# Kernel tuning notes

Hardware: AMD Instinct MI355X
Metric: run time of the kernel (lower is better)

Reference implementation:

```python
import jax, jax.numpy as jnp
import numpy as np

B, C, H, W = 8, 192, 128, 128
FILTERS = (1, 3, 3, 3, 3, 1)
BOUND = 1e-9


def setup_inputs() -> dict:
    key = jax.random.key(0)
    ks = jax.random.split(key, 16)
    d = {"x": jax.random.normal(ks[0], (B, C, H, W), jnp.float32)}
    for i in range(5):
        d[f"m{i}"] = jax.random.normal(ks[1 + i], (C, FILTERS[i + 1], FILTERS[i]), jnp.float32) * 0.5
        d[f"b{i}"] = jax.random.uniform(ks[6 + i], (C, FILTERS[i + 1], 1), jnp.float32, -0.5, 0.5)
    for i in range(4):
        d[f"f{i}"] = jax.random.normal(ks[11 + i], (C, FILTERS[i + 1], 1), jnp.float32) * 0.1
    return d


def _logits_cumulative(x, ms, bs, fs):
    # x: (C, 1, N); per-channel tiny MLP: matmul(softplus(M), x) + b, tanh gate
    logits = x
    for i in range(5):
        logits = jnp.matmul(jax.nn.softplus(ms[i]), logits) + bs[i]
        if i < 4:
            logits = logits + jnp.tanh(fs[i]) * jnp.tanh(logits)
    return logits


def reference(x, m0, m1, m2, m3, m4, b0, b1, b2, b3, b4, f0, f1, f2, f3):
    ms = (m0, m1, m2, m3, m4)
    bs = (b0, b1, b2, b3, b4)
    fs = (f0, f1, f2, f3)
    # quantize: per-sample min/max over (C,H,W), round to 16-bit grid
    x_min = jnp.min(x, axis=(1, 2, 3), keepdims=True)
    x_max = jnp.max(x, axis=(1, 2, 3), keepdims=True)
    xq = jnp.round((x - x_min) * 65535.0 / (x_max - x_min + 1e-12))
    xd = xq / 65535.0  # dequantize
    # permute (B,C,H,W)->(C,B,H,W), reshape to (C,1,N)
    xp = jnp.transpose(xd, (1, 0, 2, 3)).reshape(C, 1, -1)
    lower = _logits_cumulative(xp - 0.5, ms, bs, fs)
    upper = _logits_cumulative(xp + 0.5, ms, bs, fs)
    likelihood = jax.nn.sigmoid(upper) - jax.nn.sigmoid(lower)
    likelihood = jnp.maximum(likelihood, BOUND)  # LowerBound forward
    x_out = jnp.transpose(xp.reshape(C, B, H, W), (1, 0, 2, 3))
    likelihood = jnp.transpose(likelihood.reshape(C, B, H, W), (1, 0, 2, 3))
    return (x_out, likelihood)
```

## Files before the change

### kernel.cpp

```cpp
#include <hip/hip_runtime.h>
#include <math.h>

#define CCH 192
#define BATCH 8
#define HWSZ 16384
#define NPER (CCH * HWSZ)
#define NTOT ((size_t)BATCH * NPER)
#define INV65535 (1.0f / 65535.0f)

#define TABN    8193
#define TABSTR  8196
#define TSCALE  (8192.0f / 65535.0f)

#define WS_PMN_OFF_FLOATS  64
#define WS_PMX_OFF_FLOATS  2048
#define WS_WTAB_OFF_FLOATS 4096
#define WS_TAB_OFF_BYTES   65536
#define WS_NEEDED (WS_TAB_OFF_BYTES + (size_t)CCH * TABSTR * 4)

#define RED_BLOCKS_PER_SAMPLE 192
#define MINMAX_BLOCKS (BATCH * RED_BLOCKS_PER_SAMPLE)
#define TAB_BLOCKS (CCH * 33)

typedef float f4 __attribute__((ext_vector_type(4)));

__device__ __forceinline__ float fexp2(float x) { return __builtin_amdgcn_exp2f(x); }
__device__ __forceinline__ float frcp(float x)  { return __builtin_amdgcn_rcpf(x); }
__device__ __forceinline__ float ftanh(float x) {
    return 1.0f - 2.0f * frcp(fexp2(2.8853900817779268f * x) + 1.0f);
}
__device__ __forceinline__ float fsig(float x) {
    return frcp(1.0f + fexp2(-1.4426950408889634f * x));
}

__device__ __forceinline__ float eval_mlp(float x, const float* W)
{
    float a0 = fmaf(W[0], x, W[33]);
    float a1 = fmaf(W[1], x, W[34]);
    float a2 = fmaf(W[2], x, W[35]);
    a0 = fmaf(W[46], ftanh(a0), a0);
    a1 = fmaf(W[47], ftanh(a1), a1);
    a2 = fmaf(W[48], ftanh(a2), a2);

    float c0 = fmaf(W[3], a0, fmaf(W[4],  a1, fmaf(W[5],  a2, W[36])));
    float c1 = fmaf(W[6], a0, fmaf(W[7],  a1, fmaf(W[8],  a2, W[37])));
    float c2 = fmaf(W[9], a0, fmaf(W[10], a1, fmaf(W[11], a2, W[38])));
    c0 = fmaf(W[49], ftanh(c0), c0);
    c1 = fmaf(W[50], ftanh(c1), c1);
    c2 = fmaf(W[51], ftanh(c2), c2);

    float d0 = fmaf(W[12], c0, fmaf(W[13], c1, fmaf(W[14], c2, W[39])));
    float d1 = fmaf(W[15], c0, fmaf(W[16], c1, fmaf(W[17], c2, W[40])));
    float d2 = fmaf(W[18], c0, fmaf(W[19], c1, fmaf(W[20], c2, W[41])));
    d0 = fmaf(W[52], ftanh(d0), d0);
    d1 = fmaf(W[53], ftanh(d1), d1);
    d2 = fmaf(W[54], ftanh(d2), d2);

    float e0 = fmaf(W[21], d0, fmaf(W[22], d1, fmaf(W[23], d2, W[42])));
    float e1 = fmaf(W[24], d0, fmaf(W[25], d1, fmaf(W[26], d2, W[43])));
    float e2 = fmaf(W[27], d0, fmaf(W[28], d1, fmaf(W[29], d2, W[44])));
    e0 = fmaf(W[55], ftanh(e0), e0);
    e1 = fmaf(W[56], ftanh(e1), e1);
    e2 = fmaf(W[57], ftanh(e2), e2);

    return fmaf(W[30], e0, fmaf(W[31], e1, fmaf(W[32], e2, W[45])));
}

__device__ __forceinline__ float eval_lik(float d, const float* W)
{
    float lo = eval_mlp(d - 0.5f, W);
    float up = eval_mlp(d + 0.5f, W);
    return fmaxf(fsig(up) - fsig(lo), 1e-9f);
}

__device__ __forceinline__ void minmax_block(const float* __restrict__ x,
                                             float* __restrict__ pmn,
                                             float* __restrict__ pmx,
                                             int bid)
{
    int b   = bid / RED_BLOCKS_PER_SAMPLE;
    int blk = bid % RED_BLOCKS_PER_SAMPLE;
    const f4* xs = (const f4*)(x + (size_t)b * NPER);
    int base = blk * 4096;
    float mn = INFINITY, mx = -INFINITY;
    #pragma unroll
    for (int i = 0; i < 16; ++i) {
        f4 v = xs[base + i * 256 + threadIdx.x];
        mn = fminf(mn, fminf(fminf(v.x, v.y), fminf(v.z, v.w)));
        mx = fmaxf(mx, fmaxf(fmaxf(v.x, v.y), fmaxf(v.z, v.w)));
    }
    #pragma unroll
    for (int off = 32; off > 0; off >>= 1) {
        mn = fminf(mn, __shfl_down(mn, off, 64));
        mx = fmaxf(mx, __shfl_down(mx, off, 64));
    }
    __shared__ float smn[4], smx[4];
    int wave = threadIdx.x >> 6;
    if ((threadIdx.x & 63) == 0) { smn[wave] = mn; smx[wave] = mx; }
    __syncthreads();
    if (threadIdx.x == 0) {
        #pragma unroll
        for (int i = 1; i < 4; ++i) { mn = fminf(mn, smn[i]); mx = fmaxf(mx, smx[i]); }
        pmn[bid] = mn;
        pmx[bid] = mx;
    }
}

__global__ __launch_bounds__(256) void prep_kernel(
    const float* __restrict__ x,
    float* __restrict__ pmn, float* __restrict__ pmx,
    const float* __restrict__ m0, const float* __restrict__ b0,
    const float* __restrict__ m1, const float* __restrict__ b1,
    const float* __restrict__ m2, const float* __restrict__ b2,
    const float* __restrict__ m3, const float* __restrict__ b3,
    const float* __restrict__ m4, const float* __restrict__ b4,
    const float* __restrict__ f0, const float* __restrict__ f1,
    const float* __restrict__ f2, const float* __restrict__ f3,
    float* __restrict__ tab)
{
    if (blockIdx.x < MINMAX_BLOCKS) {
        minmax_block(x, pmn, pmx, blockIdx.x);
        return;
    }
    int tb = blockIdx.x - MINMAX_BLOCKS;
    int c  = tb / 33;
    int jc = tb % 33;
    int t  = threadIdx.x;

    __shared__ float sW[58];
    if (t < 58) {
        float v;
        if (t < 33) {
            if      (t < 3)  v = m0[c * 3 + t];
            else if (t < 12) v = m1[c * 9 + t - 3];
            else if (t < 21) v = m2[c * 9 + t - 12];
            else if (t < 30) v = m3[c * 9 + t - 21];
            else             v = m4[c * 3 + t - 30];
            v = fmaxf(v, 0.f) + log1pf(expf(-fabsf(v)));
        } else if (t < 46) {
            int i = t - 33;
            if      (i < 3)  v = b0[c * 3 + i];
            else if (i < 6)  v = b1[c * 3 + i - 3];
            else if (i < 9)  v = b2[c * 3 + i - 6];
            else if (i < 12) v = b3[c * 3 + i - 9];
            else             v = b4[c];
        } else {
            int i = t - 46;
            if      (i < 3)  v = f0[c * 3 + i];
            else if (i < 6)  v = f1[c * 3 + i - 3];
            else if (i < 9)  v = f2[c * 3 + i - 6];
            else             v = f3[c * 3 + i - 9];
            v = tanhf(v);
        }
        sW[t] = v;
    }
    __syncthreads();

    float W[58];
    #pragma unroll
    for (int i = 0; i < 58; ++i) W[i] = sW[i];

    int j = jc * 256 + t;
    if (j < TABN) {
        float d = (float)j * (1.0f / 8192.0f);
        tab[(size_t)c * TABSTR + j] = eval_lik(d, W);
    }
}

__global__ __launch_bounds__(256) void gather_kernel(const float* __restrict__ x,
                                                     const float* __restrict__ pmn,
                                                     const float* __restrict__ pmx,
                                                     const float* __restrict__ tab,
                                                     float* __restrict__ out)
{
    __shared__ __align__(16) float ltab[TABN + 3];
    __shared__ float red[4][4];

    int c  = blockIdx.x >> 2;
    int p  = blockIdx.x & 3;
    int b0 = p;
    int b1 = p + 4;
    int t  = threadIdx.x;

    size_t base0 = ((size_t)b0 * CCH + c) * HWSZ;
    size_t base1 = ((size_t)b1 * CCH + c) * HWSZ;
    const f4* xin0 = (const f4*)(x + base0);
    const f4* xin1 = (const f4*)(x + base1);

    f4 pf0 = __builtin_nontemporal_load(&xin0[t]);
    f4 pf1 = __builtin_nontemporal_load(&xin1[t]);

    const f4* tsrc = (const f4*)(tab + (size_t)c * TABSTR);
    f4* tdst = (f4*)ltab;
    #pragma unroll
    for (int i = 0; i < 8; ++i) tdst[i * 256 + t] = tsrc[i * 256 + t];
    if (t == 0) ltab[8192] = tab[(size_t)c * TABSTR + 8192];

    float mn0 = t < 192 ? pmn[b0 * RED_BLOCKS_PER_SAMPLE + t] :  INFINITY;
    float mx0 = t < 192 ? pmx[b0 * RED_BLOCKS_PER_SAMPLE + t] : -INFINITY;
    float mn1 = t < 192 ? pmn[b1 * RED_BLOCKS_PER_SAMPLE + t] :  INFINITY;
    float mx1 = t < 192 ? pmx[b1 * RED_BLOCKS_PER_SAMPLE + t] : -INFINITY;
    #pragma unroll
    for (int off = 32; off > 0; off >>= 1) {
        mn0 = fminf(mn0, __shfl_down(mn0, off, 64));
        mx0 = fmaxf(mx0, __shfl_down(mx0, off, 64));
        mn1 = fminf(mn1, __shfl_down(mn1, off, 64));
        mx1 = fmaxf(mx1, __shfl_down(mx1, off, 64));
    }
    int wave = t >> 6;
    if ((t & 63) == 0) {
        red[wave][0] = mn0; red[wave][1] = mx0;
        red[wave][2] = mn1; red[wave][3] = mx1;
    }
    __syncthreads();

    mn0 = fminf(fminf(red[0][0], red[1][0]), fminf(red[2][0], red[3][0]));
    mx0 = fmaxf(fmaxf(red[0][1], red[1][1]), fmaxf(red[2][1], red[3][1]));
    mn1 = fminf(fminf(red[0][2], red[1][2]), fminf(red[2][2], red[3][2]));
    mx1 = fmaxf(fmaxf(red[0][3], red[1][3]), fmaxf(red[2][3], red[3][3]));
    float scale0 = 65535.0f / (mx0 - mn0 + 1e-12f);
    float scale1 = 65535.0f / (mx1 - mn1 + 1e-12f);

    auto proc = [&](float xi, float mn, float scale, float& od, float& ol) {
        float kf   = rintf((xi - mn) * scale);
        od         = kf * INV65535;
        float tpos = kf * TSCALE;
        int   j    = (int)tpos;
        j = j > 8191 ? 8191 : j;
        float frac = tpos - (float)j;
        float t0 = ltab[j];
        float t1 = ltab[j + 1];
        ol = fmaxf(fmaf(frac, t1 - t0, t0), 1e-9f);
    };

    auto plane = [&](const f4* xin, f4* o0, f4* o1, float mn, float scale, f4 pf) {
        #pragma unroll
        for (int i = 0; i < 16; ++i) {
            f4 v = (i == 0) ? pf : __builtin_nontemporal_load(&xin[i * 256 + t]);
            float in[4] = {v.x, v.y, v.z, v.w};
            float xd[4], lk[4];
            #pragma unroll
            for (int k = 0; k < 4; ++k) proc(in[k], mn, scale, xd[k], lk[k]);
            f4 vxd = {xd[0], xd[1], xd[2], xd[3]};
            f4 vlk = {lk[0], lk[1], lk[2], lk[3]};
            __builtin_nontemporal_store(vxd, &o0[i * 256 + t]);
            __builtin_nontemporal_store(vlk, &o1[i * 256 + t]);
        }
    };

    plane(xin0, (f4*)(out + base0), (f4*)(out + NTOT + base0), mn0, scale0, pf0);
    plane(xin1, (f4*)(out + base1), (f4*)(out + NTOT + base1), mn1, scale1, pf1);
}

__global__ void setup_kernel(const float* __restrict__ m0, const float* __restrict__ b0,
                             const float* __restrict__ m1, const float* __restrict__ b1,
                             const float* __restrict__ m2, const float* __restrict__ b2,
                             const float* __restrict__ m3, const float* __restrict__ b3,
                             const float* __restrict__ m4, const float* __restrict__ b4,
                             const float* __restrict__ f0, const float* __restrict__ f1,
                             const float* __restrict__ f2, const float* __restrict__ f3,
                             float* __restrict__ wtab)
{
    int t = threadIdx.x;
    if (t < CCH) {
        float* w = wtab + t * 64;
        #pragma unroll
        for (int i = 0; i < 3; ++i) { float v = m0[t*3+i]; w[i]    = fmaxf(v,0.f)+log1pf(expf(-fabsf(v))); }
        #pragma unroll
        for (int i = 0; i < 9; ++i) { float v = m1[t*9+i]; w[3+i]  = fmaxf(v,0.f)+log1pf(expf(-fabsf(v))); }
        #pragma unroll
        for (int i = 0; i < 9; ++i) { float v = m2[t*9+i]; w[12+i] = fmaxf(v,0.f)+log1pf(expf(-fabsf(v))); }
        #pragma unroll
        for (int i = 0; i < 9; ++i) { float v = m3[t*9+i]; w[21+i] = fmaxf(v,0.f)+log1pf(expf(-fabsf(v))); }
        #pragma unroll
        for (int i = 0; i < 3; ++i) { float v = m4[t*3+i]; w[30+i] = fmaxf(v,0.f)+log1pf(expf(-fabsf(v))); }
        #pragma unroll
        for (int i = 0; i < 3; ++i) w[33+i] = b0[t*3+i];
        #pragma unroll
        for (int i = 0; i < 3; ++i) w[36+i] = b1[t*3+i];
        #pragma unroll
        for (int i = 0; i < 3; ++i) w[39+i] = b2[t*3+i];
        #pragma unroll
        for (int i = 0; i < 3; ++i) w[42+i] = b3[t*3+i];
        w[45] = b4[t];
        #pragma unroll
        for (int i = 0; i < 3; ++i) w[46+i] = tanhf(f0[t*3+i]);
        #pragma unroll
        for (int i = 0; i < 3; ++i) w[49+i] = tanhf(f1[t*3+i]);
        #pragma unroll
        for (int i = 0; i < 3; ++i) w[52+i] = tanhf(f2[t*3+i]);
        #pragma unroll
        for (int i = 0; i < 3; ++i) w[55+i] = tanhf(f3[t*3+i]);
    }
}

__global__ __launch_bounds__(256) void ebott_main(const float* __restrict__ x,
                                                  const float* __restrict__ pmn,
                                                  const float* __restrict__ pmx,
                                                  const float* __restrict__ wtab,
                                                  float* __restrict__ out)
{
    int blk = blockIdx.x;
    int q   = blk & 3;
    int c   = (blk >> 2) % CCH;
    int b   = blk / (4 * CCH);

    float W[58];
    const float* w = wtab + c * 64;
    #pragma unroll
    for (int i = 0; i < 58; ++i) W[i] = w[i];

    float mn = INFINITY, mx = -INFINITY;
    for (int i = 0; i < RED_BLOCKS_PER_SAMPLE; ++i) {
        mn = fminf(mn, pmn[b * RED_BLOCKS_PER_SAMPLE + i]);
        mx = fmaxf(mx, pmx[b * RED_BLOCKS_PER_SAMPLE + i]);
    }
    float scale = 65535.0f / (mx - mn + 1e-12f);

    size_t base = (size_t)(b * CCH + c) * HWSZ + q * 4096;
    const f4* xin = (const f4*)(x + base);
    f4* o0 = (f4*)(out + base);
    f4* o1 = (f4*)(out + NTOT + base);
    int t = threadIdx.x;

    #pragma unroll
    for (int i = 0; i < 4; ++i) {
        f4 v = xin[i * 256 + t];
        float in[4] = {v.x, v.y, v.z, v.w};
        float xd[4], lk[4];
        #pragma unroll
        for (int k = 0; k < 4; ++k) {
            float d = rintf((in[k] - mn) * scale) * INV65535;
            xd[k] = d;
            lk[k] = eval_lik(d, W);
        }
        f4 vxd = {xd[0], xd[1], xd[2], xd[3]};
        f4 vlk = {lk[0], lk[1], lk[2], lk[3]};
        o0[i * 256 + t] = vxd;
        o1[i * 256 + t] = vlk;
    }
}

extern "C" void kernel_launch(void* const* d_in, const int* in_sizes, int n_in,
                              void* d_out, int out_size, void* d_ws, size_t ws_size,
                              hipStream_t stream)
{
    const float* x  = (const float*)d_in[0];
    const float* m0 = (const float*)d_in[1];
    const float* b0 = (const float*)d_in[2];
    const float* m1 = (const float*)d_in[3];
    const float* b1 = (const float*)d_in[4];
    const float* m2 = (const float*)d_in[5];
    const float* b2 = (const float*)d_in[6];
    const float* m3 = (const float*)d_in[7];
    const float* b3 = (const float*)d_in[8];
    const float* m4 = (const float*)d_in[9];
    const float* b4 = (const float*)d_in[10];
    const float* f0 = (const float*)d_in[11];
    const float* f1 = (const float*)d_in[12];
    const float* f2 = (const float*)d_in[13];
    const float* f3 = (const float*)d_in[14];

    float* pmn  = (float*)d_ws + WS_PMN_OFF_FLOATS;
    float* pmx  = (float*)d_ws + WS_PMX_OFF_FLOATS;
    float* wtab = (float*)d_ws + WS_WTAB_OFF_FLOATS;
    float* tab  = (float*)((char*)d_ws + WS_TAB_OFF_BYTES);
    float* out  = (float*)d_out;

    if (ws_size >= WS_NEEDED) {
        prep_kernel<<<MINMAX_BLOCKS + TAB_BLOCKS, 256, 0, stream>>>(
            x, pmn, pmx, m0, b0, m1, b1, m2, b2, m3, b3, m4, b4, f0, f1, f2, f3, tab);
        gather_kernel<<<CCH * 4, 256, 0, stream>>>(x, pmn, pmx, tab, out);
    } else {
        setup_kernel<<<1, 256, 0, stream>>>(m0, b0, m1, b1, m2, b2, m3, b3, m4, b4,
                                            f0, f1, f2, f3, wtab);
        prep_kernel<<<MINMAX_BLOCKS, 256, 0, stream>>>(
            x, pmn, pmx, m0, b0, m1, b1, m2, b2, m3, b3, m4, b4, f0, f1, f2, f3, tab);
        ebott_main<<<BATCH * CCH * 4, 256, 0, stream>>>(x, pmn, pmx, wtab, out);
    }
}
```

Before: 324.3 us.

## Fuse minmax, table build and gather into one cooperative kernel with grid sync

Replaces the two-kernel scheme (prep with minmax plus global table, then gather) with a single cooperative kernel. Each block builds its channel's likelihood table directly in LDS while reducing min/max over its own planes, then a grid-wide sync makes the per-sample extrema visible before the gather. This removes the global table round-trip and one launch, and overlaps table evaluation with the minmax read pass. The cost is a grid barrier and reduced occupancy limits; a two-kernel fallback is kept for devices without cooperative launch.

```diff
diff --git a/kernel.cpp b/kernel.cpp
--- a/kernel.cpp
+++ b/kernel.cpp
@@ -1,5 +1,8 @@
 #include <hip/hip_runtime.h>
+#include <hip/hip_cooperative_groups.h>
 #include <math.h>
+
+namespace cg = cooperative_groups;
 
 #define CCH 192
 #define BATCH 8
@@ -9,18 +12,13 @@
 #define INV65535 (1.0f / 65535.0f)
 
 #define TABN    8193
-#define TABSTR  8196
 #define TSCALE  (8192.0f / 65535.0f)
 
-#define WS_PMN_OFF_FLOATS  64
-#define WS_PMX_OFF_FLOATS  2048
-#define WS_WTAB_OFF_FLOATS 4096
-#define WS_TAB_OFF_BYTES   65536
-#define WS_NEEDED (WS_TAB_OFF_BYTES + (size_t)CCH * TABSTR * 4)
-
-#define RED_BLOCKS_PER_SAMPLE 192
-#define MINMAX_BLOCKS (BATCH * RED_BLOCKS_PER_SAMPLE)
-#define TAB_BLOCKS (CCH * 33)
+#define WS_PMN_OFF 64
+#define WS_PMX_OFF 2112
+#define WS_NEEDED  ((size_t)(WS_PMX_OFF + BATCH * CCH) * 4)
+
+#define NBLK (CCH * 4)
 
 typedef float f4 __attribute__((ext_vector_type(4)));
 
@@ -73,61 +71,15 @@
     return fmaxf(fsig(up) - fsig(lo), 1e-9f);
 }
 
-__device__ __forceinline__ void minmax_block(const float* __restrict__ x,
-                                             float* __restrict__ pmn,
-                                             float* __restrict__ pmx,
-                                             int bid)
-{
-    int b   = bid / RED_BLOCKS_PER_SAMPLE;
-    int blk = bid % RED_BLOCKS_PER_SAMPLE;
-    const f4* xs = (const f4*)(x + (size_t)b * NPER);
-    int base = blk * 4096;
-    float mn = INFINITY, mx = -INFINITY;
-    #pragma unroll
-    for (int i = 0; i < 16; ++i) {
-        f4 v = xs[base + i * 256 + threadIdx.x];
-        mn = fminf(mn, fminf(fminf(v.x, v.y), fminf(v.z, v.w)));
-        mx = fmaxf(mx, fmaxf(fmaxf(v.x, v.y), fmaxf(v.z, v.w)));
-    }
-    #pragma unroll
-    for (int off = 32; off > 0; off >>= 1) {
-        mn = fminf(mn, __shfl_down(mn, off, 64));
-        mx = fmaxf(mx, __shfl_down(mx, off, 64));
-    }
-    __shared__ float smn[4], smx[4];
-    int wave = threadIdx.x >> 6;
-    if ((threadIdx.x & 63) == 0) { smn[wave] = mn; smx[wave] = mx; }
-    __syncthreads();
-    if (threadIdx.x == 0) {
-        #pragma unroll
-        for (int i = 1; i < 4; ++i) { mn = fminf(mn, smn[i]); mx = fmaxf(mx, smx[i]); }
-        pmn[bid] = mn;
-        pmx[bid] = mx;
-    }
-}
-
-__global__ __launch_bounds__(256) void prep_kernel(
-    const float* __restrict__ x,
-    float* __restrict__ pmn, float* __restrict__ pmx,
+__device__ __forceinline__ void stage_weights(int c, int t, float* sW,
     const float* __restrict__ m0, const float* __restrict__ b0,
     const float* __restrict__ m1, const float* __restrict__ b1,
     const float* __restrict__ m2, const float* __restrict__ b2,
     const float* __restrict__ m3, const float* __restrict__ b3,
     const float* __restrict__ m4, const float* __restrict__ b4,
     const float* __restrict__ f0, const float* __restrict__ f1,
-    const float* __restrict__ f2, const float* __restrict__ f3,
-    float* __restrict__ tab)
-{
-    if (blockIdx.x < MINMAX_BLOCKS) {
-        minmax_block(x, pmn, pmx, blockIdx.x);
-        return;
-    }
-    int tb = blockIdx.x - MINMAX_BLOCKS;
-    int c  = tb / 33;
-    int jc = tb % 33;
-    int t  = threadIdx.x;
-
-    __shared__ float sW[58];
+    const float* __restrict__ f2, const float* __restrict__ f3)
+{
     if (t < 58) {
         float v;
         if (t < 33) {
@@ -154,52 +106,128 @@
         }
         sW[t] = v;
     }
-    __syncthreads();
-
-    float W[58];
-    #pragma unroll
-    for (int i = 0; i < 58; ++i) W[i] = sW[i];
-
-    int j = jc * 256 + t;
-    if (j < TABN) {
-        float d = (float)j * (1.0f / 8192.0f);
-        tab[(size_t)c * TABSTR + j] = eval_lik(d, W);
-    }
-}
-
-__global__ __launch_bounds__(256) void gather_kernel(const float* __restrict__ x,
-                                                     const float* __restrict__ pmn,
-                                                     const float* __restrict__ pmx,
-                                                     const float* __restrict__ tab,
-                                                     float* __restrict__ out)
-{
-    __shared__ __align__(16) float ltab[TABN + 3];
-    __shared__ float red[4][4];
-
-    int c  = blockIdx.x >> 2;
-    int p  = blockIdx.x & 3;
-    int b0 = p;
-    int b1 = p + 4;
-    int t  = threadIdx.x;
-
-    size_t base0 = ((size_t)b0 * CCH + c) * HWSZ;
-    size_t base1 = ((size_t)b1 * CCH + c) * HWSZ;
+}
+
+__device__ __forceinline__ void gather_plane(const f4* __restrict__ xin,
+                                             f4* __restrict__ o0, f4* __restrict__ o1,
+                                             float mn, float scale,
+                                             const float* ltab, int t, f4 pf)
+{
+    #pragma unroll
+    for (int i = 0; i < 16; ++i) {
+        f4 v = (i == 0) ? pf : xin[i * 256 + t];
+        float in[4] = {v.x, v.y, v.z, v.w};
+        float xd[4], lk[4];
+        #pragma unroll
+        for (int k = 0; k < 4; ++k) {
+            float kf   = rintf((in[k] - mn) * scale);
+            xd[k]      = kf * INV65535;
+            float tpos = kf * TSCALE;
+            int   j    = (int)tpos;
+            j = j > 8191 ? 8191 : j;
+            float frac = tpos - (float)j;
+            float t0 = ltab[j];
+            float t1 = ltab[j + 1];
+            lk[k] = fmaxf(fmaf(frac, t1 - t0, t0), 1e-9f);
+        }
+        f4 vxd = {xd[0], xd[1], xd[2], xd[3]};
+        f4 vlk = {lk[0], lk[1], lk[2], lk[3]};
+        __builtin_nontemporal_store(vxd, &o0[i * 256 + t]);
+        __builtin_nontemporal_store(vlk, &o1[i * 256 + t]);
+    }
+}
+
+__device__ __forceinline__ void phase2_gather(
+    const float* __restrict__ x, const float* __restrict__ pmn,
+    const float* __restrict__ pmx, float* __restrict__ out,
+    const float* ltab, float (*red)[4], int c, int p, int t)
+{
+    int s0 = p, s1 = p + 4;
+    size_t base0 = ((size_t)s0 * CCH + c) * HWSZ;
+    size_t base1 = ((size_t)s1 * CCH + c) * HWSZ;
     const f4* xin0 = (const f4*)(x + base0);
     const f4* xin1 = (const f4*)(x + base1);
 
-    f4 pf0 = __builtin_nontemporal_load(&xin0[t]);
-    f4 pf1 = __builtin_nontemporal_load(&xin1[t]);
-
-    const f4* tsrc = (const f4*)(tab + (size_t)c * TABSTR);
-    f4* tdst = (f4*)ltab;
-    #pragma unroll
-    for (int i = 0; i < 8; ++i) tdst[i * 256 + t] = tsrc[i * 256 + t];
-    if (t == 0) ltab[8192] = tab[(size_t)c * TABSTR + 8192];
-
-    float mn0 = t < 192 ? pmn[b0 * RED_BLOCKS_PER_SAMPLE + t] :  INFINITY;
-    float mx0 = t < 192 ? pmx[b0 * RED_BLOCKS_PER_SAMPLE + t] : -INFINITY;
-    float mn1 = t < 192 ? pmn[b1 * RED_BLOCKS_PER_SAMPLE + t] :  INFINITY;
-    float mx1 = t < 192 ? pmx[b1 * RED_BLOCKS_PER_SAMPLE + t] : -INFINITY;
+    f4 pf0 = xin0[t];
+    f4 pf1 = xin1[t];
+
+    float amn0 = t < CCH ? pmn[s0 * CCH + t] :  INFINITY;
+    float amx0 = t < CCH ? pmx[s0 * CCH + t] : -INFINITY;
+    float amn1 = t < CCH ? pmn[s1 * CCH + t] :  INFINITY;
+    float amx1 = t < CCH ? pmx[s1 * CCH + t] : -INFINITY;
+    #pragma unroll
+    for (int off = 32; off > 0; off >>= 1) {
+        amn0 = fminf(amn0, __shfl_down(amn0, off, 64));
+        amx0 = fmaxf(amx0, __shfl_down(amx0, off, 64));
+        amn1 = fminf(amn1, __shfl_down(amn1, off, 64));
+        amx1 = fmaxf(amx1, __shfl_down(amx1, off, 64));
+    }
+    int wave = t >> 6;
+    if ((t & 63) == 0) {
+        red[wave][0] = amn0; red[wave][1] = amx0;
+        red[wave][2] = amn1; red[wave][3] = amx1;
+    }
+    __syncthreads();
+    float mn0 = fminf(fminf(red[0][0], red[1][0]), fminf(red[2][0], red[3][0]));
+    float mx0 = fmaxf(fmaxf(red[0][1], red[1][1]), fmaxf(red[2][1], red[3][1]));
+    float mn1 = fminf(fminf(red[0][2], red[1][2]), fminf(red[2][2], red[3][2]));
+    float mx1 = fmaxf(fmaxf(red[0][3], red[1][3]), fmaxf(red[2][3], red[3][3]));
+    float sc0 = 65535.0f / (mx0 - mn0 + 1e-12f);
+    float sc1 = 65535.0f / (mx1 - mn1 + 1e-12f);
+
+    gather_plane(xin0, (f4*)(out + base0), (f4*)(out + NTOT + base0), mn0, sc0, ltab, t, pf0);
+    gather_plane(xin1, (f4*)(out + base1), (f4*)(out + NTOT + base1), mn1, sc1, ltab, t, pf1);
+}
+
+__global__ __launch_bounds__(256, 3) void fused_kernel(
+    const float* __restrict__ x,
+    float* __restrict__ pmn, float* __restrict__ pmx,
+    float* __restrict__ out,
+    const float* __restrict__ m0, const float* __restrict__ b0,
+    const float* __restrict__ m1, const float* __restrict__ b1,
+    const float* __restrict__ m2, const float* __restrict__ b2,
+    const float* __restrict__ m3, const float* __restrict__ b3,
+    const float* __restrict__ m4, const float* __restrict__ b4,
+    const float* __restrict__ f0, const float* __restrict__ f1,
+    const float* __restrict__ f2, const float* __restrict__ f3)
+{
+    __shared__ __align__(16) float ltab[TABN + 3];
+    __shared__ float sW[58];
+    __shared__ float red[4][4];
+
+    int c = blockIdx.x >> 2;
+    int p = blockIdx.x & 3;
+    int s0 = p, s1 = p + 4;
+    int t = threadIdx.x;
+
+    stage_weights(c, t, sW, m0, b0, m1, b1, m2, b2, m3, b3, m4, b4, f0, f1, f2, f3);
+    __syncthreads();
+
+    float W[58];
+    #pragma unroll
+    for (int i = 0; i < 58; ++i) W[i] = sW[i];
+
+    size_t base0 = ((size_t)s0 * CCH + c) * HWSZ;
+    size_t base1 = ((size_t)s1 * CCH + c) * HWSZ;
+    const f4* xin0 = (const f4*)(x + base0);
+    const f4* xin1 = (const f4*)(x + base1);
+
+    float mn0 = INFINITY, mx0 = -INFINITY, mn1 = INFINITY, mx1 = -INFINITY;
+
+    #pragma unroll 2
+    for (int it = 0; it < 16; ++it) {
+        f4 v0 = xin0[it * 256 + t];
+        f4 v1 = xin1[it * 256 + t];
+        int j = it * 512 + t;
+        ltab[j]       = eval_lik((float)j * (1.0f / 8192.0f), W);
+        ltab[j + 256] = eval_lik((float)(j + 256) * (1.0f / 8192.0f), W);
+        mn0 = fminf(mn0, fminf(fminf(v0.x, v0.y), fminf(v0.z, v0.w)));
+        mx0 = fmaxf(mx0, fmaxf(fmaxf(v0.x, v0.y), fmaxf(v0.z, v0.w)));
+        mn1 = fminf(mn1, fminf(fminf(v1.x, v1.y), fminf(v1.z, v1.w)));
+        mx1 = fmaxf(mx1, fmaxf(fmaxf(v1.x, v1.y), fmaxf(v1.z, v1.w)));
+    }
+    if (t == 0) ltab[8192] = eval_lik(1.0f, W);
+
     #pragma unroll
     for (int off = 32; off > 0; off >>= 1) {
         mn0 = fminf(mn0, __shfl_down(mn0, off, 64));
@@ -213,132 +241,86 @@
         red[wave][2] = mn1; red[wave][3] = mx1;
     }
     __syncthreads();
-
-    mn0 = fminf(fminf(red[0][0], red[1][0]), fminf(red[2][0], red[3][0]));
-    mx0 = fmaxf(fmaxf(red[0][1], red[1][1]), fmaxf(red[2][1], red[3][1]));
-    mn1 = fminf(fminf(red[0][2], red[1][2]), fminf(red[2][2], red[3][2]));
-    mx1 = fmaxf(fmaxf(red[0][3], red[1][3]), fmaxf(red[2][3], red[3][3]));
-    float scale0 = 65535.0f / (mx0 - mn0 + 1e-12f);
-    float scale1 = 65535.0f / (mx1 - mn1 + 1e-12f);
-
-    auto proc = [&](float xi, float mn, float scale, float& od, float& ol) {
-        float kf   = rintf((xi - mn) * scale);
-        od         = kf * INV65535;
-        float tpos = kf * TSCALE;
-        int   j    = (int)tpos;
-        j = j > 8191 ? 8191 : j;
-        float frac = tpos - (float)j;
-        float t0 = ltab[j];
-        float t1 = ltab[j + 1];
-        ol = fmaxf(fmaf(frac, t1 - t0, t0), 1e-9f);
-    };
-
-    auto plane = [&](const f4* xin, f4* o0, f4* o1, float mn, float scale, f4 pf) {
+    if (t == 0) {
         #pragma unroll
-        for (int i = 0; i < 16; ++i) {
-            f4 v = (i == 0) ? pf : __builtin_nontemporal_load(&xin[i * 256 + t]);
-            float in[4] = {v.x, v.y, v.z, v.w};
-            float xd[4], lk[4];
-            #pragma unroll
-            for (int k = 0; k < 4; ++k) proc(in[k], mn, scale, xd[k], lk[k]);
-            f4 vxd = {xd[0], xd[1], xd[2], xd[3]};
-            f4 vlk = {lk[0], lk[1], lk[2], lk[3]};
-            __builtin_nontemporal_store(vxd, &o0[i * 256 + t]);
-            __builtin_nontemporal_store(vlk, &o1[i * 256 + t]);
+        for (int i = 1; i < 4; ++i) {
+            mn0 = fminf(mn0, red[i][0]); mx0 = fmaxf(mx0, red[i][1]);
+            mn1 = fminf(mn1, red[i][2]); mx1 = fmaxf(mx1, red[i][3]);
         }
-    };
-
-    plane(xin0, (f4*)(out + base0), (f4*)(out + NTOT + base0), mn0, scale0, pf0);
-    plane(xin1, (f4*)(out + base1), (f4*)(out + NTOT + base1), mn1, scale1, pf1);
-}
-
-__global__ void setup_kernel(const float* __restrict__ m0, const float* __restrict__ b0,
-                             const float* __restrict__ m1, const float* __restrict__ b1,
-                             const float* __restrict__ m2, const float* __restrict__ b2,
-                             const float* __restrict__ m3, const float* __restrict__ b3,
-                             const float* __restrict__ m4, const float* __restrict__ b4,
-                             const float* __restrict__ f0, const float* __restrict__ f1,
-                             const float* __restrict__ f2, const float* __restrict__ f3,
-                             float* __restrict__ wtab)
-{
+        pmn[s0 * CCH + c] = mn0; pmx[s0 * CCH + c] = mx0;
+        pmn[s1 * CCH + c] = mn1; pmx[s1 * CCH + c] = mx1;
+    }
+    __threadfence();
+    cg::this_grid().sync();
+
+    phase2_gather(x, pmn, pmx, out, ltab, red, c, p, t);
+}
+
+__global__ __launch_bounds__(256) void minmax_kernel(const float* __restrict__ x,
+                                                     float* __restrict__ pmn,
+                                                     float* __restrict__ pmx)
+{
+    const f4* xs = (const f4*)(x + (size_t)blockIdx.x * HWSZ);
     int t = threadIdx.x;
-    if (t < CCH) {
-        float* w = wtab + t * 64;
+    float mn = INFINITY, mx = -INFINITY;
+    #pragma unroll
+    for (int i = 0; i < 16; ++i) {
+        f4 v = xs[i * 256 + t];
+        mn = fminf(mn, fminf(fminf(v.x, v.y), fminf(v.z, v.w)));
+        mx = fmaxf(mx, fmaxf(fmaxf(v.x, v.y), fmaxf(v.z, v.w)));
+    }
+    #pragma unroll
+    for (int off = 32; off > 0; off >>= 1) {
+        mn = fminf(mn, __shfl_down(mn, off, 64));
+        mx = fmaxf(mx, __shfl_down(mx, off, 64));
+    }
+    __shared__ float smn[4], smx[4];
+    int wave = t >> 6;
+    if ((t & 63) == 0) { smn[wave] = mn; smx[wave] = mx; }
+    __syncthreads();
+    if (t == 0) {
         #pragma unroll
-        for (int i = 0; i < 3; ++i) { float v = m0[t*3+i]; w[i]    = fmaxf(v,0.f)+log1pf(expf(-fabsf(v))); }
-        #pragma unroll
-        for (int i = 0; i < 9; ++i) { float v = m1[t*9+i]; w[3+i]  = fmaxf(v,0.f)+log1pf(expf(-fabsf(v))); }
-        #pragma unroll
-        for (int i = 0; i < 9; ++i) { float v = m2[t*9+i]; w[12+i] = fmaxf(v,0.f)+log1pf(expf(-fabsf(v))); }
-        #pragma unroll
-        for (int i = 0; i < 9; ++i) { float v = m3[t*9+i]; w[21+i] = fmaxf(v,0.f)+log1pf(expf(-fabsf(v))); }
-        #pragma unroll
-        for (int i = 0; i < 3; ++i) { float v = m4[t*3+i]; w[30+i] = fmaxf(v,0.f)+log1pf(expf(-fabsf(v))); }
-        #pragma unroll
-        for (int i = 0; i < 3; ++i) w[33+i] = b0[t*3+i];
-        #pragma unroll
-        for (int i = 0; i < 3; ++i) w[36+i] = b1[t*3+i];
-        #pragma unroll
-        for (int i = 0; i < 3; ++i) w[39+i] = b2[t*3+i];
-        #pragma unroll
-        for (int i = 0; i < 3; ++i) w[42+i] = b3[t*3+i];
-        w[45] = b4[t];
-        #pragma unroll
-        for (int i = 0; i < 3; ++i) w[46+i] = tanhf(f0[t*3+i]);
-        #pragma unroll
-        for (int i = 0; i < 3; ++i) w[49+i] = tanhf(f1[t*3+i]);
-        #pragma unroll
-        for (int i = 0; i < 3; ++i) w[52+i] = tanhf(f2[t*3+i]);
-        #pragma unroll
-        for (int i = 0; i < 3; ++i) w[55+i] = tanhf(f3[t*3+i]);
-    }
-}
-
-__global__ __launch_bounds__(256) void ebott_main(const float* __restrict__ x,
-                                                  const float* __restrict__ pmn,
-                                                  const float* __restrict__ pmx,
-                                                  const float* __restrict__ wtab,
-                                                  float* __restrict__ out)
-{
-    int blk = blockIdx.x;
-    int q   = blk & 3;
-    int c   = (blk >> 2) % CCH;
-    int b   = blk / (4 * CCH);
+        for (int i = 1; i < 4; ++i) { mn = fminf(mn, smn[i]); mx = fmaxf(mx, smx[i]); }
+        pmn[blockIdx.x] = mn;
+        pmx[blockIdx.x] = mx;
+    }
+}
+
+__global__ __launch_bounds__(256, 3) void gather_local_kernel(
+    const float* __restrict__ x,
+    const float* __restrict__ pmn, const float* __restrict__ pmx,
+    const float* __restrict__ m0, const float* __restrict__ b0,
+    const float* __restrict__ m1, const float* __restrict__ b1,
+    const float* __restrict__ m2, const float* __restrict__ b2,
+    const float* __restrict__ m3, const float* __restrict__ b3,
+    const float* __restrict__ m4, const float* __restrict__ b4,
+    const float* __restrict__ f0, const float* __restrict__ f1,
+    const float* __restrict__ f2, const float* __restrict__ f3,
+    float* __restrict__ out)
+{
+    __shared__ __align__(16) float ltab[TABN + 3];
+    __shared__ float sW[58];
+    __shared__ float red[4][4];
+
+    int c = blockIdx.x >> 2;
+    int p = blockIdx.x & 3;
+    int t = threadIdx.x;
+
+    stage_weights(c, t, sW, m0, b0, m1, b1, m2, b2, m3, b3, m4, b4, f0, f1, f2, f3);
+    __syncthreads();
 
     float W[58];
-    const float* w = wtab + c * 64;
-    #pragma unroll
-    for (int i = 0; i < 58; ++i) W[i] = w[i];
-
-    float mn = INFINITY, mx = -INFINITY;
-    for (int i = 0; i < RED_BLOCKS_PER_SAMPLE; ++i) {
-        mn = fminf(mn, pmn[b * RED_BLOCKS_PER_SAMPLE + i]);
-        mx = fmaxf(mx, pmx[b * RED_BLOCKS_PER_SAMPLE + i]);
-    }
-    float scale = 65535.0f / (mx - mn + 1e-12f);
-
-    size_t base = (size_t)(b * CCH + c) * HWSZ + q * 4096;
-    const f4* xin = (const f4*)(x + base);
-    f4* o0 = (f4*)(out + base);
-    f4* o1 = (f4*)(out + NTOT + base);
-    int t = threadIdx.x;
-
-    #pragma unroll
-    for (int i = 0; i < 4; ++i) {
-        f4 v = xin[i * 256 + t];
-        float in[4] = {v.x, v.y, v.z, v.w};
-        float xd[4], lk[4];
-        #pragma unroll
-        for (int k = 0; k < 4; ++k) {
-            float d = rintf((in[k] - mn) * scale) * INV65535;
-            xd[k] = d;
-            lk[k] = eval_lik(d, W);
-        }
-        f4 vxd = {xd[0], xd[1], xd[2], xd[3]};
-        f4 vlk = {lk[0], lk[1], lk[2], lk[3]};
-        o0[i * 256 + t] = vxd;
-        o1[i * 256 + t] = vlk;
-    }
+    #pragma unroll
+    for (int i = 0; i < 58; ++i) W[i] = sW[i];
+
+    #pragma unroll 2
+    for (int it = 0; it < 32; ++it) {
+        int j = it * 256 + t;
+        ltab[j] = eval_lik((float)j * (1.0f / 8192.0f), W);
+    }
+    if (t == 0) ltab[8192] = eval_lik(1.0f, W);
+
+    phase2_gather(x, pmn, pmx, out, ltab, red, c, p, t);
 }
 
 extern "C" void kernel_launch(void* const* d_in, const int* in_sizes, int n_in,
@@ -361,21 +343,30 @@
     const float* f2 = (const float*)d_in[13];
     const float* f3 = (const float*)d_in[14];
 
-    float* pmn  = (float*)d_ws + WS_PMN_OFF_FLOATS;
-    float* pmx  = (float*)d_ws + WS_PMX_OFF_FLOATS;
-    float* wtab = (float*)d_ws + WS_WTAB_OFF_FLOATS;
-    float* tab  = (float*)((char*)d_ws + WS_TAB_OFF_BYTES);
-    float* out  = (float*)d_out;
-
-    if (ws_size >= WS_NEEDED) {
-        prep_kernel<<<MINMAX_BLOCKS + TAB_BLOCKS, 256, 0, stream>>>(
-            x, pmn, pmx, m0, b0, m1, b1, m2, b2, m3, b3, m4, b4, f0, f1, f2, f3, tab);
-        gather_kernel<<<CCH * 4, 256, 0, stream>>>(x, pmn, pmx, tab, out);
-    } else {
-        setup_kernel<<<1, 256, 0, stream>>>(m0, b0, m1, b1, m2, b2, m3, b3, m4, b4,
-                                            f0, f1, f2, f3, wtab);
-        prep_kernel<<<MINMAX_BLOCKS, 256, 0, stream>>>(
-            x, pmn, pmx, m0, b0, m1, b1, m2, b2, m3, b3, m4, b4, f0, f1, f2, f3, tab);
-        ebott_main<<<BATCH * CCH * 4, 256, 0, stream>>>(x, pmn, pmx, wtab, out);
-    }
-}
+    float* pmn = (float*)d_ws + WS_PMN_OFF;
+    float* pmx = (float*)d_ws + WS_PMX_OFF;
+    float* out = (float*)d_out;
+
+    static int coop_ok = -1;
+    if (coop_ok < 0) {
+        int dev = 0, v = 0;
+        hipGetDevice(&dev);
+        if (hipDeviceGetAttribute(&v, hipDeviceAttributeCooperativeLaunch, dev) != hipSuccess) v = 0;
+        coop_ok = v;
+    }
+
+    if (coop_ok) {
+        void* kargs[] = {(void*)&x, (void*)&pmn, (void*)&pmx, (void*)&out,
+                         (void*)&m0, (void*)&b0, (void*)&m1, (void*)&b1,
+                         (void*)&m2, (void*)&b2, (void*)&m3, (void*)&b3,
+                         (void*)&m4, (void*)&b4, (void*)&f0, (void*)&f1,
+                         (void*)&f2, (void*)&f3};
+        if (hipLaunchCooperativeKernel((const void*)fused_kernel, dim3(NBLK), dim3(256),
+                                       kargs, 0, stream) == hipSuccess)
+            return;
+    }
+
+    minmax_kernel<<<BATCH * CCH, 256, 0, stream>>>(x, pmn, pmx);
+    gather_local_kernel<<<NBLK, 256, 0, stream>>>(x, pmn, pmx,
+        m0, b0, m1, b1, m2, b2, m3, b3, m4, b4, f0, f1, f2, f3, out);
+}
```

Measured after the change: 503.7 us. 55.3% more time.
